# Performance work log

Measured on AMD Instinct MI355X. Metric: run time of the kernel, lower is better.

## Reference

```python
import jax, jax.numpy as jnp
import numpy as np


def setup_inputs() -> dict:
    key = jax.random.key(0)
    k1, k2, k3, k4, k5 = jax.random.split(key, 5)
    B, C, T, U = 4, 256, 4096, 64
    y1 = jax.random.normal(k1, (B, C, T), dtype=jnp.float32)
    y2 = jax.random.normal(k2, (B, C, T), dtype=jnp.float32)
    # module init: uniform(-0.02, 0.02)
    Wq = jax.random.uniform(k3, (C, U), minval=-0.02, maxval=0.02, dtype=jnp.float32)
    Wk = jax.random.uniform(k4, (C, U), minval=-0.02, maxval=0.02, dtype=jnp.float32)
    Wv = jax.random.uniform(k5, (C, U), minval=-0.02, maxval=0.02, dtype=jnp.float32)
    return {"y1": y1, "y2": y2, "Wq": Wq, "Wk": Wk, "Wv": Wv, "attention_width": 256}


def reference(y1, y2, Wq, Wk, Wv, attention_width):
    # y1, y2: [B, C, T] -> projected to [B, T, U]
    q1 = jnp.einsum('bct,cu->btu', y1, Wq)
    k2 = jnp.einsum('bct,cu->btu', y2, Wk)
    v2 = jnp.einsum('bct,cu->btu', y2, Wv)
    d_k = q1.shape[-1]
    # scores e[b, i, j] = q1[b,i,:] . k2[b,j,:] / sqrt(U)
    e = jnp.einsum('biu,bju->bij', q1, k2) / jnp.sqrt(jnp.float32(d_k))
    T = e.shape[-1]
    # banded mask: keep (i, j) where j - w//2 <= i < j - w//2 + w
    lower = jnp.arange(T) - attention_width // 2          # [T] (per column j)
    upper = lower + attention_width                        # [T]
    i = jnp.arange(T)[:, None]                             # [T, 1] (row index)
    mask = (lower <= i) & (i < upper)                      # [T, T]
    e = jnp.where(mask, e, -jnp.inf)
    a = jax.nn.softmax(e, axis=-1)                         # [B, T, T]
    # out = (a @ v2) then permute(0, 2, 1) -> [B, U, T]
    out = jnp.einsum('bij,bju->bui', a, v2)
    return (out, a)
```

## Files before the change

kernel.cpp:

```cpp
#include <hip/hip_runtime.h>

using uint = unsigned int;
typedef unsigned short ushort_t;
typedef float f32x4 __attribute__((ext_vector_type(4)));
typedef short short8 __attribute__((ext_vector_type(8)));

#define B_ 4
#define C_ 256
#define T_ 4096
#define U_ 64

static __device__ __forceinline__ float bflo(uint w) { return __uint_as_float(w << 16); }
static __device__ __forceinline__ float bfhi(uint w) { return __uint_as_float(w & 0xffff0000u); }
static __device__ __forceinline__ uint f2bf(float f) {
    uint x = __float_as_uint(f);
    return (x + 0x7fffu + ((x >> 16) & 1u)) >> 16;
}

__global__ __launch_bounds__(256) void proj_kernel(
    const float* __restrict__ y1, const float* __restrict__ y2,
    const float* __restrict__ Wq, const float* __restrict__ Wk,
    const float* __restrict__ Wv,
    ushort_t* __restrict__ Qb, ushort_t* __restrict__ Kb, ushort_t* __restrict__ Vb)
{
    __shared__ alignas(16) ushort_t wt[2][64][264];

    const int p   = blockIdx.y;
    const int b   = blockIdx.x >> 6;
    const int t0  = (blockIdx.x & 63) << 6;
    const int tid = threadIdx.x;

    {
        const float* W0 = (p == 0) ? Wq : Wk;
#pragma unroll
        for (int k = 0; k < 64; ++k) {
            int idx = tid + 256 * k;
            int c = idx >> 6, u = idx & 63;
            wt[0][u][c] = (ushort_t)f2bf(W0[idx]);
        }
        if (p == 1) {
#pragma unroll
            for (int k = 0; k < 64; ++k) {
                int idx = tid + 256 * k;
                int c = idx >> 6, u = idx & 63;
                wt[1][u][c] = (ushort_t)f2bf(Wv[idx]);
            }
        }
    }
    __syncthreads();

    const int wid = tid >> 6, l = tid & 63;
    const int lm = l & 15, lg = l >> 4;

    const float* ysrc = ((p == 0) ? y1 : y2) + (size_t)b * (C_ * T_);
    const float* yp   = ysrc + (size_t)(8 * lg) * T_ + (t0 + 16 * wid + lm);

    float avf[8][8];
#pragma unroll
    for (int ks = 0; ks < 8; ++ks)
#pragma unroll
        for (int j = 0; j < 8; ++j)
            avf[ks][j] = yp[(size_t)(32 * ks + j) * T_];

    short8 afr[8];
#pragma unroll
    for (int ks = 0; ks < 8; ++ks)
#pragma unroll
        for (int j = 0; j < 8; ++j)
            afr[ks][j] = (short)f2bf(avf[ks][j]);

    f32x4 acc0[4] = {};
    f32x4 acc1[4] = {};
#pragma unroll
    for (int ks = 0; ks < 8; ++ks) {
#pragma unroll
        for (int n = 0; n < 4; ++n) {
            short8 bq = *(const short8*)&wt[0][16 * n + lm][32 * ks + 8 * lg];
            acc0[n] = __builtin_amdgcn_mfma_f32_16x16x32_bf16(afr[ks], bq, acc0[n], 0, 0, 0);
            if (p == 1) {
                short8 bv = *(const short8*)&wt[1][16 * n + lm][32 * ks + 8 * lg];
                acc1[n] = __builtin_amdgcn_mfma_f32_16x16x32_bf16(afr[ks], bv, acc1[n], 0, 0, 0);
            }
        }
    }

    ushort_t* O0 = (p == 0) ? Qb : Kb;
#pragma unroll
    for (int n = 0; n < 4; ++n)
#pragma unroll
        for (int r = 0; r < 4; ++r) {
            int t = t0 + 16 * wid + 4 * lg + r;
            int u = 16 * n + lm;
            size_t off = ((size_t)b * T_ + t) * 64 + u;
            O0[off] = (ushort_t)f2bf(acc0[n][r]);
            if (p == 1) Vb[off] = (ushort_t)f2bf(acc1[n][r]);
        }
}

__global__ __launch_bounds__(256, 2) void attn_kernel(
    const uint* __restrict__ Qb, const uint* __restrict__ Kb,
    const uint* __restrict__ Vb, float* __restrict__ gout)
{
    __shared__ alignas(16) uint kw[271 * 32];
    __shared__ alignas(16) uint vw[271 * 32];
    __shared__ float   qlds[16][64];
    __shared__ ushort_t alds[4][256];
    __shared__ float   olds[64][17];

    const int bid = blockIdx.x;
    const int b   = bid >> 8;
    const int i0  = (bid & 255) << 4;
    const int tid = threadIdx.x;

    const int jb    = max(0, i0 - 127);
    const int jend  = min(T_, i0 + 16 + 128);
    const int width = jend - jb;

    {
        const uint4* ks = (const uint4*)(Kb + ((size_t)b * T_ + jb) * 32);
        const uint4* vs = (const uint4*)(Vb + ((size_t)b * T_ + jb) * 32);
        int n4 = width * 8;
        for (int idx = tid; idx < n4; idx += 256) {
            int row  = idx >> 3;
            int q4   = (idx & 7) << 2;
            int phys = q4 ^ ((row & 7) << 2);
            *(uint4*)&kw[row * 32 + phys] = ks[idx];
            *(uint4*)&vw[row * 32 + phys] = vs[idx];
        }
    }
    {
        const uint* qs = Qb + ((size_t)b * T_ + i0) * 32;
        for (int idx = tid; idx < 512; idx += 256) {
            uint w = qs[idx];
            float2 f; f.x = bflo(w); f.y = bfhi(w);
            ((float2*)qlds)[idx] = f;
        }
    }
    __syncthreads();

    const int wv = tid >> 6;
    const int l  = tid & 63;
    float* aout = gout + (size_t)B_ * U_ * T_;

    for (int rr = 0; rr < 4; ++rr) {
        const int r = 4 * wv + rr;
        const int i = i0 + r;
        const int jlo = max(0, i - 127);
        const int jhi = min(T_ - 1, i + 128);
        float* rowp = aout + ((size_t)(b * T_ + i)) * T_;
        f32x4* row4 = (f32x4*)rowp;

        const int rowoff = jlo - jb;
        int jlbase[4], sel[4];
        bool valid[4];
#pragma unroll
        for (int p = 0; p < 4; ++p) {
            int joff = l + 64 * p;
            valid[p] = (jlo + joff) <= jhi;
            int t = rowoff + joff;
            if (t > width - 1) t = width - 1;
            jlbase[p] = t * 32;
            sel[p]    = (t & 7) << 2;
        }
        float S[4] = {0.f, 0.f, 0.f, 0.f};
#pragma unroll
        for (int m = 0; m < 8; ++m) {
            float4 q0 = *(float4*)&qlds[r][8 * m];
            float4 q1 = *(float4*)&qlds[r][8 * m + 4];
#pragma unroll
            for (int p = 0; p < 4; ++p) {
                uint4 kk = *(uint4*)&kw[jlbase[p] + ((4 * m) ^ sel[p])];
                float s = S[p];
                s = fmaf(q0.x, bflo(kk.x), s);  s = fmaf(q0.y, bfhi(kk.x), s);
                s = fmaf(q0.z, bflo(kk.y), s);  s = fmaf(q0.w, bfhi(kk.y), s);
                s = fmaf(q1.x, bflo(kk.z), s);  s = fmaf(q1.y, bfhi(kk.z), s);
                s = fmaf(q1.z, bflo(kk.w), s);  s = fmaf(q1.w, bfhi(kk.w), s);
                S[p] = s;
            }
        }

        float e[4], esum = 0.f;
#pragma unroll
        for (int p = 0; p < 4; ++p) {
            e[p] = valid[p] ? __expf(S[p] * 0.125f) : 0.f;
            esum += e[p];
        }
#pragma unroll
        for (int d = 1; d < 64; d <<= 1)
            esum += __shfl_xor(esum, d, 64);
        float rinv = __builtin_amdgcn_rcpf(esum);
        float av[4];
#pragma unroll
        for (int p = 0; p < 4; ++p) av[p] = e[p] * rinv;

#pragma unroll
        for (int p = 0; p < 4; ++p) {
            if (valid[p])
                __builtin_nontemporal_store(av[p], rowp + jlo + l + 64 * p);
            alds[wv][l + 64 * p] = (ushort_t)f2bf(av[p]);
        }
        {
            f32x4 z = (f32x4)(0.f);
            int nleft4 = jlo >> 2;
            for (int k = l; k < nleft4; k += 64)
                __builtin_nontemporal_store(z, row4 + k);
            int rem = jlo & 3;
            if (l < rem)
                __builtin_nontemporal_store(0.f, rowp + (jlo & ~3) + l);
            int js = jhi + 1;
            int ah = (4 - (js & 3)) & 3;
            if (l < ah)
                __builtin_nontemporal_store(0.f, rowp + js + l);
            int js4 = (js + ah) >> 2;
            for (int k = js4 + l; k < T_ / 4; k += 64)
                __builtin_nontemporal_store(z, row4 + k);
        }
        asm volatile("s_waitcnt lgkmcnt(0)" ::: "memory");

        {
            const int jq = l >> 4, uq = l & 15;
            float o0 = 0.f, o1 = 0.f, o2 = 0.f, o3 = 0.f;
#pragma unroll 8
            for (int jj = 0; jj < 64; ++jj) {
                int joff = 4 * jj + jq;
                float aw = __uint_as_float(((uint)alds[wv][joff]) << 16);
                int t = rowoff + joff;
                if (t > width - 1) t = width - 1;
                uint2 vv = *(uint2*)&vw[t * 32 + ((2 * uq) ^ ((t & 7) << 2))];
                o0 = fmaf(aw, bflo(vv.x), o0);
                o1 = fmaf(aw, bfhi(vv.x), o1);
                o2 = fmaf(aw, bflo(vv.y), o2);
                o3 = fmaf(aw, bfhi(vv.y), o3);
            }
            o0 += __shfl_xor(o0, 16, 64);  o0 += __shfl_xor(o0, 32, 64);
            o1 += __shfl_xor(o1, 16, 64);  o1 += __shfl_xor(o1, 32, 64);
            o2 += __shfl_xor(o2, 16, 64);  o2 += __shfl_xor(o2, 32, 64);
            o3 += __shfl_xor(o3, 16, 64);  o3 += __shfl_xor(o3, 32, 64);
            if (l < 16) {
                olds[4 * uq + 0][r] = o0;
                olds[4 * uq + 1][r] = o1;
                olds[4 * uq + 2][r] = o2;
                olds[4 * uq + 3][r] = o3;
            }
        }
    }
    __syncthreads();

    {
        const int u = tid >> 2, e4 = tid & 3;
        f32x4 o;
        o.x = olds[u][4 * e4 + 0];
        o.y = olds[u][4 * e4 + 1];
        o.z = olds[u][4 * e4 + 2];
        o.w = olds[u][4 * e4 + 3];
        __builtin_nontemporal_store(o, (f32x4*)(gout + ((size_t)b * U_ + u) * T_ + i0 + 4 * e4));
    }
}

extern "C" void kernel_launch(void* const* d_in, const int* in_sizes, int n_in,
                              void* d_out, int out_size, void* d_ws, size_t ws_size,
                              hipStream_t stream)
{
    const float* y1 = (const float*)d_in[0];
    const float* y2 = (const float*)d_in[1];
    const float* Wq = (const float*)d_in[2];
    const float* Wk = (const float*)d_in[3];
    const float* Wv = (const float*)d_in[4];

    ushort_t* Qb = (ushort_t*)d_ws;
    ushort_t* Kb = Qb + (size_t)B_ * T_ * 64;
    ushort_t* Vb = Kb + (size_t)B_ * T_ * 64;

    float* gout = (float*)d_out;

    dim3 g1(B_ * (T_ / 64), 2);
    proj_kernel<<<g1, 256, 0, stream>>>(y1, y2, Wq, Wk, Wv, Qb, Kb, Vb);

    attn_kernel<<<dim3(B_ * (T_ / 16)), 256, 0, stream>>>(
        (const uint*)Qb, (const uint*)Kb, (const uint*)Vb, gout);
}
```

Measured before the change: 84.61 us.

## Move attention-matrix zero fill into projection kernel and pretranspose weights

A small kernel now converts and transposes the weights to bf16 once, so the projection kernel reads them from global memory instead of rebuilding them in LDS in every block. The projection kernel also zero-fills the whole 256 MB attention matrix, overlapping that write with its y1/y2 reads; the attention kernel then writes only the banded entries, which overwrite the zeros. The A·V inner loop uses 8-wide V loads with fewer iterations, and nontemporal stores become plain stores. The cost is a full-matrix zero pass followed by the band writes, which correctness depends on running in stream order, plus an extra kernel launch.

```diff
diff --git a/kernel.cpp b/kernel.cpp
--- a/kernel.cpp
+++ b/kernel.cpp
@@ -17,83 +17,81 @@
     return (x + 0x7fffu + ((x >> 16) & 1u)) >> 16;
 }
 
+__global__ __launch_bounds__(256) void wconv_kernel(
+    const float* __restrict__ Wq, const float* __restrict__ Wk,
+    const float* __restrict__ Wv, ushort_t* __restrict__ WT)
+{
+    const int m = blockIdx.x >> 3;
+    const int q = blockIdx.x & 7;
+    const float* W = (m == 0) ? Wq : (m == 1) ? Wk : Wv;
+    int g  = q * 256 + threadIdx.x;
+    int u  = g >> 5;
+    int c8 = (g & 31) << 3;
+    short8 o;
+#pragma unroll
+    for (int j = 0; j < 8; ++j)
+        o[j] = (short)f2bf(W[(size_t)(c8 + j) * U_ + u]);
+    *(short8*)(WT + ((size_t)m * U_ + u) * C_ + c8) = o;
+}
+
 __global__ __launch_bounds__(256) void proj_kernel(
     const float* __restrict__ y1, const float* __restrict__ y2,
-    const float* __restrict__ Wq, const float* __restrict__ Wk,
-    const float* __restrict__ Wv,
-    ushort_t* __restrict__ Qb, ushort_t* __restrict__ Kb, ushort_t* __restrict__ Vb)
-{
-    __shared__ alignas(16) ushort_t wt[2][64][264];
-
-    const int p   = blockIdx.y;
-    const int b   = blockIdx.x >> 6;
-    const int t0  = (blockIdx.x & 63) << 6;
+    const ushort_t* __restrict__ WT,
+    ushort_t* __restrict__ Qb, ushort_t* __restrict__ Kb, ushort_t* __restrict__ Vb,
+    float* __restrict__ azero)
+{
+    const int bid = blockIdx.x;
+    const int p   = bid & 1;
+    const int bq2 = bid >> 1;
+    const int b   = bq2 >> 6;
+    const int t0  = (bq2 & 63) << 6;
     const int tid = threadIdx.x;
-
-    {
-        const float* W0 = (p == 0) ? Wq : Wk;
-#pragma unroll
-        for (int k = 0; k < 64; ++k) {
-            int idx = tid + 256 * k;
-            int c = idx >> 6, u = idx & 63;
-            wt[0][u][c] = (ushort_t)f2bf(W0[idx]);
-        }
-        if (p == 1) {
-#pragma unroll
-            for (int k = 0; k < 64; ++k) {
-                int idx = tid + 256 * k;
-                int c = idx >> 6, u = idx & 63;
-                wt[1][u][c] = (ushort_t)f2bf(Wv[idx]);
-            }
-        }
-    }
-    __syncthreads();
-
     const int wid = tid >> 6, l = tid & 63;
-    const int lm = l & 15, lg = l >> 4;
+    const int lm  = l & 15, lg = l >> 4;
 
     const float* ysrc = ((p == 0) ? y1 : y2) + (size_t)b * (C_ * T_);
     const float* yp   = ysrc + (size_t)(8 * lg) * T_ + (t0 + 16 * wid + lm);
-
-    float avf[8][8];
-#pragma unroll
-    for (int ks = 0; ks < 8; ++ks)
-#pragma unroll
-        for (int j = 0; j < 8; ++j)
-            avf[ks][j] = yp[(size_t)(32 * ks + j) * T_];
-
-    short8 afr[8];
-#pragma unroll
-    for (int ks = 0; ks < 8; ++ks)
-#pragma unroll
-        for (int j = 0; j < 8; ++j)
-            afr[ks][j] = (short)f2bf(avf[ks][j]);
+    const ushort_t* WT0 = WT + (size_t)(p == 0 ? 0 : 1) * (U_ * C_);
+    const ushort_t* WT1 = WT + (size_t)2 * (U_ * C_);
+
+    f32x4* zb = (f32x4*)azero + (size_t)bid * 32768 + tid;
+    const f32x4 zz = (f32x4)(0.f);
 
     f32x4 acc0[4] = {};
     f32x4 acc1[4] = {};
 #pragma unroll
     for (int ks = 0; ks < 8; ++ks) {
+        float av[8];
+#pragma unroll
+        for (int j = 0; j < 8; ++j)
+            av[j] = yp[(size_t)(32 * ks + j) * T_];
+        short8 af;
+#pragma unroll
+        for (int j = 0; j < 8; ++j)
+            af[j] = (short)f2bf(av[j]);
 #pragma unroll
         for (int n = 0; n < 4; ++n) {
-            short8 bq = *(const short8*)&wt[0][16 * n + lm][32 * ks + 8 * lg];
-            acc0[n] = __builtin_amdgcn_mfma_f32_16x16x32_bf16(afr[ks], bq, acc0[n], 0, 0, 0);
-            if (p == 1) {
-                short8 bv = *(const short8*)&wt[1][16 * n + lm][32 * ks + 8 * lg];
-                acc1[n] = __builtin_amdgcn_mfma_f32_16x16x32_bf16(afr[ks], bv, acc1[n], 0, 0, 0);
-            }
-        }
-    }
-
-    ushort_t* O0 = (p == 0) ? Qb : Kb;
+            short8 bq = *(const short8*)(WT0 + (size_t)(16 * n + lm) * C_ + 32 * ks + 8 * lg);
+            acc0[n] = __builtin_amdgcn_mfma_f32_16x16x32_bf16(af, bq, acc0[n], 0, 0, 0);
+            if (p) {
+                short8 bv = *(const short8*)(WT1 + (size_t)(16 * n + lm) * C_ + 32 * ks + 8 * lg);
+                acc1[n] = __builtin_amdgcn_mfma_f32_16x16x32_bf16(af, bv, acc1[n], 0, 0, 0);
+            }
+        }
+#pragma unroll
+        for (int z = 0; z < 16; ++z)
+            zb[256 * (16 * ks + z)] = zz;
+    }
+
+    ushort_t* O0 = p ? Kb : Qb;
 #pragma unroll
     for (int n = 0; n < 4; ++n)
 #pragma unroll
         for (int r = 0; r < 4; ++r) {
             int t = t0 + 16 * wid + 4 * lg + r;
-            int u = 16 * n + lm;
-            size_t off = ((size_t)b * T_ + t) * 64 + u;
+            size_t off = ((size_t)b * T_ + t) * U_ + 16 * n + lm;
             O0[off] = (ushort_t)f2bf(acc0[n][r]);
-            if (p == 1) Vb[off] = (ushort_t)f2bf(acc1[n][r]);
+            if (p) Vb[off] = (ushort_t)f2bf(acc1[n][r]);
         }
 }
 
@@ -148,7 +146,6 @@
         const int jlo = max(0, i - 127);
         const int jhi = min(T_ - 1, i + 128);
         float* rowp = aout + ((size_t)(b * T_ + i)) * T_;
-        f32x4* row4 = (f32x4*)rowp;
 
         const int rowoff = jlo - jb;
         int jlbase[4], sel[4];
@@ -196,52 +193,40 @@
 #pragma unroll
         for (int p = 0; p < 4; ++p) {
             if (valid[p])
-                __builtin_nontemporal_store(av[p], rowp + jlo + l + 64 * p);
+                rowp[jlo + l + 64 * p] = av[p];
             alds[wv][l + 64 * p] = (ushort_t)f2bf(av[p]);
         }
+        asm volatile("s_waitcnt lgkmcnt(0)" ::: "memory");
+
         {
-            f32x4 z = (f32x4)(0.f);
-            int nleft4 = jlo >> 2;
-            for (int k = l; k < nleft4; k += 64)
-                __builtin_nontemporal_store(z, row4 + k);
-            int rem = jlo & 3;
-            if (l < rem)
-                __builtin_nontemporal_store(0.f, rowp + (jlo & ~3) + l);
-            int js = jhi + 1;
-            int ah = (4 - (js & 3)) & 3;
-            if (l < ah)
-                __builtin_nontemporal_store(0.f, rowp + js + l);
-            int js4 = (js + ah) >> 2;
-            for (int k = js4 + l; k < T_ / 4; k += 64)
-                __builtin_nontemporal_store(z, row4 + k);
-        }
-        asm volatile("s_waitcnt lgkmcnt(0)" ::: "memory");
-
-        {
-            const int jq = l >> 4, uq = l & 15;
-            float o0 = 0.f, o1 = 0.f, o2 = 0.f, o3 = 0.f;
-#pragma unroll 8
-            for (int jj = 0; jj < 64; ++jj) {
-                int joff = 4 * jj + jq;
+            const int jq = l >> 3, uo = l & 7;
+            float o[8] = {};
+#pragma unroll 4
+            for (int it = 0; it < 32; ++it) {
+                int joff = 8 * it + jq;
                 float aw = __uint_as_float(((uint)alds[wv][joff]) << 16);
                 int t = rowoff + joff;
                 if (t > width - 1) t = width - 1;
-                uint2 vv = *(uint2*)&vw[t * 32 + ((2 * uq) ^ ((t & 7) << 2))];
-                o0 = fmaf(aw, bflo(vv.x), o0);
-                o1 = fmaf(aw, bfhi(vv.x), o1);
-                o2 = fmaf(aw, bflo(vv.y), o2);
-                o3 = fmaf(aw, bfhi(vv.y), o3);
-            }
-            o0 += __shfl_xor(o0, 16, 64);  o0 += __shfl_xor(o0, 32, 64);
-            o1 += __shfl_xor(o1, 16, 64);  o1 += __shfl_xor(o1, 32, 64);
-            o2 += __shfl_xor(o2, 16, 64);  o2 += __shfl_xor(o2, 32, 64);
-            o3 += __shfl_xor(o3, 16, 64);  o3 += __shfl_xor(o3, 32, 64);
-            if (l < 16) {
-                olds[4 * uq + 0][r] = o0;
-                olds[4 * uq + 1][r] = o1;
-                olds[4 * uq + 2][r] = o2;
-                olds[4 * uq + 3][r] = o3;
-            }
+                uint4 vv = *(uint4*)&vw[t * 32 + ((4 * uo) ^ ((t & 7) << 2))];
+                o[0] = fmaf(aw, bflo(vv.x), o[0]);
+                o[1] = fmaf(aw, bfhi(vv.x), o[1]);
+                o[2] = fmaf(aw, bflo(vv.y), o[2]);
+                o[3] = fmaf(aw, bfhi(vv.y), o[3]);
+                o[4] = fmaf(aw, bflo(vv.z), o[4]);
+                o[5] = fmaf(aw, bfhi(vv.z), o[5]);
+                o[6] = fmaf(aw, bflo(vv.w), o[6]);
+                o[7] = fmaf(aw, bfhi(vv.w), o[7]);
+            }
+#pragma unroll
+            for (int k = 0; k < 8; ++k) {
+                o[k] += __shfl_xor(o[k], 8, 64);
+                o[k] += __shfl_xor(o[k], 16, 64);
+                o[k] += __shfl_xor(o[k], 32, 64);
+            }
+            if (l < 8)
+#pragma unroll
+                for (int k = 0; k < 8; ++k)
+                    olds[8 * l + k][r] = o[k];
         }
     }
     __syncthreads();
@@ -253,7 +238,7 @@
         o.y = olds[u][4 * e4 + 1];
         o.z = olds[u][4 * e4 + 2];
         o.w = olds[u][4 * e4 + 3];
-        __builtin_nontemporal_store(o, (f32x4*)(gout + ((size_t)b * U_ + u) * T_ + i0 + 4 * e4));
+        *(f32x4*)(gout + ((size_t)b * U_ + u) * T_ + i0 + 4 * e4) = o;
     }
 }
 
@@ -268,14 +253,15 @@
     const float* Wv = (const float*)d_in[4];
 
     ushort_t* Qb = (ushort_t*)d_ws;
-    ushort_t* Kb = Qb + (size_t)B_ * T_ * 64;
-    ushort_t* Vb = Kb + (size_t)B_ * T_ * 64;
+    ushort_t* Kb = Qb + (size_t)B_ * T_ * U_;
+    ushort_t* Vb = Kb + (size_t)B_ * T_ * U_;
+    ushort_t* WT = Vb + (size_t)B_ * T_ * U_;
 
     float* gout = (float*)d_out;
-
-    dim3 g1(B_ * (T_ / 64), 2);
-    proj_kernel<<<g1, 256, 0, stream>>>(y1, y2, Wq, Wk, Wv, Qb, Kb, Vb);
-
-    attn_kernel<<<dim3(B_ * (T_ / 16)), 256, 0, stream>>>(
+    float* aout = gout + (size_t)B_ * U_ * T_;
+
+    wconv_kernel<<<24, 256, 0, stream>>>(Wq, Wk, Wv, WT);
+    proj_kernel<<<512, 256, 0, stream>>>(y1, y2, WT, Qb, Kb, Vb, aout);
+    attn_kernel<<<1024, 256, 0, stream>>>(
         (const uint*)Qb, (const uint*)Kb, (const uint*)Vb, gout);
 }
```

Measured after the change: 130.7 us. 54.5% more time.
